# Performance work log

Measured on AMD Instinct MI355X. Metric: run time of the kernel, lower is better.

The kernel has to match this reference:

```python
import jax, jax.numpy as jnp
import numpy as np

M = 65536   # query points
N = 65536   # key points
K = 16      # neighbors per query
C = 64      # channels


def setup_inputs() -> dict:
    key = jax.random.key(0)
    ks = jax.random.split(key, 12)
    f = jax.random.normal
    s = 1.0 / np.sqrt(C).astype(np.float32)
    return {
        "q": f(ks[0], (M, C), dtype=jnp.float32),
        "k": f(ks[1], (N, C), dtype=jnp.float32),
        "value": f(ks[2], (M, K, C), dtype=jnp.float32),
        "q_pos": f(ks[3], (M, C), dtype=jnp.float32),
        "k_pos": f(ks[4], (N, C), dtype=jnp.float32),
        "mask": jax.random.uniform(ks[5], (M, K, 1)) < 0.1,
        "knearest_idx": jax.random.randint(ks[6], (2, M, K), 0, N),
        "k_num": K,
        # q_conv and k_conv share weights in the original module
        "Wqk": f(ks[7], (C, C), dtype=jnp.float32) * s,
        "bqk": jnp.zeros((C,), jnp.float32),
        "Wv": f(ks[8], (C, C), dtype=jnp.float32) * s,
        "bv": jnp.zeros((C,), jnp.float32),
        "Wg1": f(ks[9], (C, C), dtype=jnp.float32) * s,
        "bg1": jnp.zeros((C,), jnp.float32),
        "Wg2": f(ks[10], (C, C), dtype=jnp.float32) * s,
        "bg2": jnp.zeros((C,), jnp.float32),
        "Wt": f(ks[11], (C, C), dtype=jnp.float32) * s,
        "bt": jnp.zeros((C,), jnp.float32),
    }


def reference(q, k, value, q_pos, k_pos, mask, knearest_idx, k_num,
              Wqk, bqk, Wv, bv, Wg1, bg1, Wg2, bg2, Wt, bt):
    # shared q/k projection (tied weights) with positional add
    qp = (q + q_pos) @ Wqk + bqk            # [M, C]
    kp = (k + k_pos) @ Wqk + bqk            # [N, C]
    v = value @ Wv + bv                      # [M, K, C]
    # neighbor indices: row 1 of knearest_idx reshaped to [_, M, k_num]
    idx = knearest_idx.reshape(knearest_idx.shape[0], -1, k_num)[1]  # [M, K]
    kg = kp[idx]                              # gather -> [M, K, C]
    # per-edge MLP on q - k (fc_gamma)
    e = qp[:, None, :] - kg                   # [M, K, C]
    e = jax.nn.relu(e @ Wg1 + bg1) @ Wg2 + bg2
    e = jnp.where(mask, jnp.float32(-1e12), e)
    attn = jax.nn.softmax(e, axis=1)          # softmax over neighbor dim
    res = jnp.einsum('mnf,mnf->mf', attn, v)  # weighted aggregate -> [M, C]
    return res @ Wt + bt
```

## Files before the change

kernel.cpp:

```cpp
#include <hip/hip_runtime.h>
#include <hip/hip_bf16.h>

#define MQ 65536
#define NKEY 65536
#define KNB 16
#define CCH 64

typedef _Float16 half8  __attribute__((ext_vector_type(8)));
typedef _Float16 half4v __attribute__((ext_vector_type(4)));
typedef _Float16 half2v __attribute__((ext_vector_type(2)));
typedef float    floatx4 __attribute__((ext_vector_type(4)));


__global__ __launch_bounds__(256, 2)
void proj_prep(const float* __restrict__ q, const float* __restrict__ qpos,
               const float* __restrict__ k, const float* __restrict__ kpos,
               const float* __restrict__ Wqk, const float* __restrict__ bqk,
               const float* __restrict__ Wg1, const float* __restrict__ Wg2,
               const float* __restrict__ Wv,  const float* __restrict__ Wt,
               const unsigned char* __restrict__ maskraw,
               _Float16* __restrict__ qp_h, _Float16* __restrict__ kp_h,
               _Float16* __restrict__ w4, int* __restrict__ mflag)
{
    const int tid = threadIdx.x;

    if (blockIdx.x == 512) {
        __shared__ int sflags;
        if (tid == 0) sflags = 0;
        __syncthreads();
        const uint4* m4 = (const uint4*)maskraw;
        unsigned int orw = 0;
        #pragma unroll
        for (int it = 0; it < 4; ++it) {
            uint4 v = m4[tid + it * 256];
            orw |= v.x | v.y | v.z | v.w;
        }
        int local = 0;
        if (orw & 0x000000FFu) local |= 1;
        if (orw & 0x0000FF00u) local |= 2;
        if (orw & 0xFFFF0000u) local |= 4;
        if (local) atomicOr(&sflags, local);
        __syncthreads();
        if (tid == 0) *mflag = sflags;
        const float* Ws[4] = {Wg1, Wg2, Wv, Wt};
        #pragma unroll
        for (int mat = 0; mat < 4; ++mat) {
            const float* W = Ws[mat];
            _Float16* dst = w4 + mat * 64 * 72;
            for (int i = tid; i < 4096; i += 256) {
                int rr = i >> 6, c = i & 63;
                dst[c * 72 + rr] = (_Float16)W[i];
            }
        }
        return;
    }

    __shared__ __align__(16) _Float16 A_s[256 * 72];
    __shared__ __align__(16) _Float16 WT_s[64 * 72];

    const int r0 = blockIdx.x * 256;
    const float* x; const float* p; _Float16* o; int rb;
    if (r0 < MQ) { x = q; p = qpos; o = qp_h; rb = r0; }
    else         { x = k; p = kpos; o = kp_h; rb = r0 - MQ; }

    #pragma unroll
    for (int j = 0; j < 4; ++j) {
        int i = (tid + j * 256) * 4;
        int rr = i >> 6, c4 = i & 63;
        floatx4 wv = *(const floatx4*)&Wqk[rr * 64 + c4];
        WT_s[(c4 + 0) * 72 + rr] = (_Float16)wv.x;
        WT_s[(c4 + 1) * 72 + rr] = (_Float16)wv.y;
        WT_s[(c4 + 2) * 72 + rr] = (_Float16)wv.z;
        WT_s[(c4 + 3) * 72 + rr] = (_Float16)wv.w;
    }
    #pragma unroll
    for (int j = 0; j < 16; ++j) {
        int flat = tid + j * 256;
        int rr = flat >> 4, c4 = (flat & 15) * 4;
        size_t g = (size_t)(rb + rr) * 64 + c4;
        floatx4 xv = *(const floatx4*)&x[g];
        floatx4 pv = *(const floatx4*)&p[g];
        half4v h;
        h[0] = (_Float16)(xv.x + pv.x); h[1] = (_Float16)(xv.y + pv.y);
        h[2] = (_Float16)(xv.z + pv.z); h[3] = (_Float16)(xv.w + pv.w);
        *(half4v*)&A_s[rr * 72 + c4] = h;
    }
    __syncthreads();

    const int w = tid >> 6, lane = tid & 63, m = lane & 15, qd = lane >> 4;
    const floatx4 fz = {0.f, 0.f, 0.f, 0.f};
    floatx4 acc[4][4];
    #pragma unroll
    for (int rt = 0; rt < 4; rt++)
        #pragma unroll
        for (int ct = 0; ct < 4; ct++) acc[rt][ct] = fz;

    #pragma unroll
    for (int kc = 0; kc < 2; ++kc) {
        const int k0 = kc * 32 + qd * 8;
        half8 b[4];
        #pragma unroll
        for (int ct = 0; ct < 4; ++ct)
            b[ct] = *(const half8*)&WT_s[(ct * 16 + m) * 72 + k0];
        #pragma unroll
        for (int rt = 0; rt < 4; ++rt) {
            half8 a = *(const half8*)&A_s[(w * 64 + rt * 16 + m) * 72 + k0];
            #pragma unroll
            for (int ct = 0; ct < 4; ++ct)
                acc[rt][ct] = __builtin_amdgcn_mfma_f32_16x16x32_f16(a, b[ct], acc[rt][ct], 0, 0, 0);
        }
    }
    #pragma unroll
    for (int rt = 0; rt < 4; rt++) {
        #pragma unroll
        for (int ct = 0; ct < 4; ct++) {
            const int col = ct * 16 + m;
            const float bb = bqk[col];
            #pragma unroll
            for (int rg = 0; rg < 4; ++rg) {
                const int row = w * 64 + rt * 16 + qd * 4 + rg;
                A_s[row * 72 + col] = (_Float16)(acc[rt][ct][rg] + bb);
            }
        }
    }
    __syncthreads();
    #pragma unroll
    for (int j = 0; j < 8; ++j) {
        int ch = tid + j * 256;
        int rr = ch >> 3, off = (ch & 7) * 8;
        *(half8*)&o[(size_t)(rb + rr) * 64 + off] = *(const half8*)&A_s[rr * 72 + off];
    }
}

__global__ __launch_bounds__(256, 2)
void cross_attn(const float* __restrict__ value, const unsigned char* __restrict__ maskraw,
                const int* __restrict__ mflag, const int* __restrict__ idx,
                const _Float16* __restrict__ qp_h, const _Float16* __restrict__ kp_h,
                const _Float16* __restrict__ w4,
                const float* __restrict__ bg1, const float* __restrict__ bg2,
                const float* __restrict__ bv,  const float* __restrict__ bt,
                float* __restrict__ out)
{
    __shared__ __align__(16) _Float16 W4_s[4 * 64 * 72];
    __shared__ __align__(16) _Float16 D_s[256 * 72];
    __shared__ __align__(16) _Float16 res_s[16 * 72];
    __shared__ unsigned char mask_s[256];

    const int tid = threadIdx.x;
    const int q0 = blockIdx.x * 16;
    const int w = tid >> 6, lane = tid & 63, m = lane & 15, qd = lane >> 4;

    floatx4 vraw[16];
    {
        const size_t base = ((size_t)q0 * KNB + w * 64) * 64;
        #pragma unroll
        for (int rt = 0; rt < 4; ++rt)
            #pragma unroll
            for (int kc = 0; kc < 2; ++kc) {
                const float* vr = value + base + (size_t)(rt * 16 + m) * 64 + kc * 32 + qd * 8;
                vraw[(rt * 2 + kc) * 2 + 0] = *(const floatx4*)vr;
                vraw[(rt * 2 + kc) * 2 + 1] = *(const floatx4*)(vr + 4);
            }
    }

    #pragma unroll
    for (int j = 0; j < 9; ++j) {
        int ch = tid + j * 256;
        *(half8*)&W4_s[ch * 8] = *(const half8*)&w4[ch * 8];
    }
    {
        const int mode = *mflag;
        const size_t ei = (size_t)q0 * KNB + tid;
        unsigned char mv;
        if (mode & 2)      mv = maskraw[ei];
        else if (mode & 1) mv = ((const int*)maskraw)[ei] ? 1 : 0;
        else               mv = (((const float*)maskraw)[ei] != 0.f) ? 1 : 0;
        mask_s[tid] = mv;
    }
    {
        const int pr = tid & 31;
        #pragma unroll 8
        for (int i = 0; i < 32; ++i) {
            int e = (tid >> 5) + i * 8;
            int nb = idx[(size_t)q0 * KNB + e];
            int mrow = q0 + (e >> 4);
            half2v qv = *(const half2v*)&qp_h[(size_t)mrow * 64 + pr * 2];
            half2v kv = *(const half2v*)&kp_h[(size_t)nb * 64 + pr * 2];
            half2v d; d[0] = qv[0] - kv[0]; d[1] = qv[1] - kv[1];
            *(half2v*)&D_s[e * 72 + pr * 2] = d;
        }
    }
    __syncthreads();

    const floatx4 fz = {0.f, 0.f, 0.f, 0.f};
    float bvv[4], bg1v[4], bg2v[4];
    #pragma unroll
    for (int ct = 0; ct < 4; ct++) {
        const int col = ct * 16 + m;
        bvv[ct] = bv[col]; bg1v[ct] = bg1[col]; bg2v[ct] = bg2[col];
    }

    const _Float16* Wg1T = W4_s;
    const _Float16* Wg2T = W4_s + 4608;
    const _Float16* WvT  = W4_s + 2 * 4608;
    const _Float16* WtT  = W4_s + 3 * 4608;

    floatx4 acce[4][4];
    #pragma unroll
    for (int rt = 0; rt < 4; rt++)
        #pragma unroll
        for (int ct = 0; ct < 4; ct++) acce[rt][ct] = fz;
    #pragma unroll
    for (int kc = 0; kc < 2; ++kc) {
        const int k0 = kc * 32 + qd * 8;
        half8 b[4];
        #pragma unroll
        for (int ct = 0; ct < 4; ++ct)
            b[ct] = *(const half8*)&Wg1T[(ct * 16 + m) * 72 + k0];
        #pragma unroll
        for (int rt = 0; rt < 4; ++rt) {
            half8 a = *(const half8*)&D_s[(w * 64 + rt * 16 + m) * 72 + k0];
            #pragma unroll
            for (int ct = 0; ct < 4; ++ct)
                acce[rt][ct] = __builtin_amdgcn_mfma_f32_16x16x32_f16(a, b[ct], acce[rt][ct], 0, 0, 0);
        }
    }
    __syncthreads();
    #pragma unroll
    for (int rt = 0; rt < 4; rt++)
        #pragma unroll
        for (int ct = 0; ct < 4; ct++) {
            const int col = ct * 16 + m;
            #pragma unroll
            for (int rg = 0; rg < 4; ++rg) {
                const int row = w * 64 + rt * 16 + qd * 4 + rg;
                float h = acce[rt][ct][rg] + bg1v[ct];
                D_s[row * 72 + col] = (_Float16)fmaxf(h, 0.f);
            }
        }
    __syncthreads();

    #pragma unroll
    for (int rt = 0; rt < 4; rt++)
        #pragma unroll
        for (int ct = 0; ct < 4; ct++) acce[rt][ct] = fz;
    #pragma unroll
    for (int kc = 0; kc < 2; ++kc) {
        const int k0 = kc * 32 + qd * 8;
        half8 b[4];
        #pragma unroll
        for (int ct = 0; ct < 4; ++ct)
            b[ct] = *(const half8*)&Wg2T[(ct * 16 + m) * 72 + k0];
        #pragma unroll
        for (int rt = 0; rt < 4; ++rt) {
            half8 a = *(const half8*)&D_s[(w * 64 + rt * 16 + m) * 72 + k0];
            #pragma unroll
            for (int ct = 0; ct < 4; ++ct)
                acce[rt][ct] = __builtin_amdgcn_mfma_f32_16x16x32_f16(a, b[ct], acce[rt][ct], 0, 0, 0);
        }
    }

    half8 vfrag[8];
    #pragma unroll
    for (int f = 0; f < 8; ++f) {
        floatx4 x0 = vraw[f * 2], x1 = vraw[f * 2 + 1];
        half8 a;
        #pragma unroll
        for (int j = 0; j < 4; ++j) { a[j] = (_Float16)x0[j]; a[4 + j] = (_Float16)x1[j]; }
        vfrag[f] = a;
    }
    floatx4 accv[4][4];
    #pragma unroll
    for (int rt = 0; rt < 4; rt++)
        #pragma unroll
        for (int ct = 0; ct < 4; ct++) accv[rt][ct] = fz;
    #pragma unroll
    for (int kc = 0; kc < 2; ++kc) {
        const int k0 = kc * 32 + qd * 8;
        half8 b[4];
        #pragma unroll
        for (int ct = 0; ct < 4; ++ct)
            b[ct] = *(const half8*)&WvT[(ct * 16 + m) * 72 + k0];
        #pragma unroll
        for (int rt = 0; rt < 4; ++rt) {
            half8 a = vfrag[rt * 2 + kc];
            #pragma unroll
            for (int ct = 0; ct < 4; ++ct)
                accv[rt][ct] = __builtin_amdgcn_mfma_f32_16x16x32_f16(a, b[ct], accv[rt][ct], 0, 0, 0);
        }
    }

    #pragma unroll
    for (int rt = 0; rt < 4; rt++) {
        #pragma unroll
        for (int ct = 0; ct < 4; ct++) {
            float ev[4];
            #pragma unroll
            for (int rg = 0; rg < 4; ++rg) {
                const int erow = w * 64 + rt * 16 + qd * 4 + rg;
                float e = acce[rt][ct][rg] + bg2v[ct];
                ev[rg] = mask_s[erow] ? -1e12f : e;
            }
            float mx = fmaxf(fmaxf(ev[0], ev[1]), fmaxf(ev[2], ev[3]));
            mx = fmaxf(mx, __shfl_xor(mx, 16));
            mx = fmaxf(mx, __shfl_xor(mx, 32));
            float p[4], s = 0.f;
            #pragma unroll
            for (int rg = 0; rg < 4; ++rg) { p[rg] = __expf(ev[rg] - mx); s += p[rg]; }
            s += __shfl_xor(s, 16);
            s += __shfl_xor(s, 32);
            const float inv = 1.f / s;
            float t = 0.f;
            #pragma unroll
            for (int rg = 0; rg < 4; ++rg)
                t += p[rg] * inv * (accv[rt][ct][rg] + bvv[ct]);
            t += __shfl_xor(t, 16);
            t += __shfl_xor(t, 32);
            if (lane < 16) res_s[(w * 4 + rt) * 72 + ct * 16 + m] = (_Float16)t;
        }
    }
    __syncthreads();

    if (w == 0) {
        floatx4 acco[4] = {fz, fz, fz, fz};
        #pragma unroll
        for (int kc = 0; kc < 2; ++kc) {
            const int k0 = kc * 32 + qd * 8;
            half8 a = *(const half8*)&res_s[m * 72 + k0];
            #pragma unroll
            for (int ct = 0; ct < 4; ++ct) {
                half8 b = *(const half8*)&WtT[(ct * 16 + m) * 72 + k0];
                acco[ct] = __builtin_amdgcn_mfma_f32_16x16x32_f16(a, b, acco[ct], 0, 0, 0);
            }
        }
        #pragma unroll
        for (int ct = 0; ct < 4; ++ct) {
            const int col = ct * 16 + m;
            const float bb = bt[col];
            #pragma unroll
            for (int rg = 0; rg < 4; ++rg) {
                const int row = qd * 4 + rg;
                out[(size_t)(q0 + row) * 64 + col] = acco[ct][rg] + bb;
            }
        }
    }
}

extern "C" void kernel_launch(void* const* d_in, const int* in_sizes, int n_in,
                              void* d_out, int out_size, void* d_ws, size_t ws_size,
                              hipStream_t stream) {
    const float* q     = (const float*)d_in[0];
    const float* k     = (const float*)d_in[1];
    const float* value = (const float*)d_in[2];
    const float* q_pos = (const float*)d_in[3];
    const float* k_pos = (const float*)d_in[4];
    const unsigned char* mask = (const unsigned char*)d_in[5];
    const int* knn     = (const int*)d_in[6];
    const float* Wqk = (const float*)d_in[8];
    const float* bqk = (const float*)d_in[9];
    const float* Wv  = (const float*)d_in[10];
    const float* bv  = (const float*)d_in[11];
    const float* Wg1 = (const float*)d_in[12];
    const float* bg1 = (const float*)d_in[13];
    const float* Wg2 = (const float*)d_in[14];
    const float* bg2 = (const float*)d_in[15];
    const float* Wt  = (const float*)d_in[16];
    const float* bt  = (const float*)d_in[17];
    float* out = (float*)d_out;

    _Float16* qp_h = (_Float16*)d_ws;
    _Float16* kp_h = qp_h + (size_t)MQ * CCH;
    _Float16* w4   = kp_h + (size_t)NKEY * CCH;
    int* mflag     = (int*)(w4 + 4 * 64 * 72);
    const int* idx = knn + (size_t)MQ * KNB;

    proj_prep<<<513, 256, 0, stream>>>(q, q_pos, k, k_pos, Wqk, bqk,
                                       Wg1, Wg2, Wv, Wt, mask,
                                       qp_h, kp_h, w4, mflag);
    cross_attn<<<MQ / 16, 256, 0, stream>>>(value, mask, mflag, idx, qp_h, kp_h, w4,
                                            bg1, bg2, bv, bt, out);
}
```

Baseline: 538.0 us.

## Make cross-attention persistent over tiles with register prefetch and split out projection

New measurement: 683.6 us. +27.1%, slower.

```diff
diff --git a/kernel.cpp b/kernel.cpp
--- a/kernel.cpp
+++ b/kernel.cpp
@@ -5,60 +5,98 @@
 #define NKEY 65536
 #define KNB 16
 #define CCH 64
+#define TPB 8
 
 typedef _Float16 half8  __attribute__((ext_vector_type(8)));
 typedef _Float16 half4v __attribute__((ext_vector_type(4)));
-typedef _Float16 half2v __attribute__((ext_vector_type(2)));
 typedef float    floatx4 __attribute__((ext_vector_type(4)));
 
 
-__global__ __launch_bounds__(256, 2)
+__global__ void detect_mask(const unsigned char* __restrict__ m, int* __restrict__ flag)
+{
+    __shared__ int sflags;
+    if (threadIdx.x == 0) sflags = 0;
+    __syncthreads();
+    const uint4* m4 = (const uint4*)m;
+    unsigned int orw = 0;
+    #pragma unroll
+    for (int it = 0; it < 4; ++it) {
+        uint4 v = m4[threadIdx.x + it * 256];
+        orw |= v.x | v.y | v.z | v.w;
+    }
+    int local = 0;
+    if (orw & 0x000000FFu) local |= 1;
+    if (orw & 0x0000FF00u) local |= 2;
+    if (orw & 0xFFFF0000u) local |= 4;
+    if (local) atomicOr(&sflags, local);
+    __syncthreads();
+    if (threadIdx.x == 0) *flag = sflags;
+}
+
+__global__ __launch_bounds__(256, 4)
 void proj_prep(const float* __restrict__ q, const float* __restrict__ qpos,
                const float* __restrict__ k, const float* __restrict__ kpos,
                const float* __restrict__ Wqk, const float* __restrict__ bqk,
                const float* __restrict__ Wg1, const float* __restrict__ Wg2,
                const float* __restrict__ Wv,  const float* __restrict__ Wt,
-               const unsigned char* __restrict__ maskraw,
+               const unsigned char* __restrict__ maskraw, const int* __restrict__ mflag,
                _Float16* __restrict__ qp_h, _Float16* __restrict__ kp_h,
-               _Float16* __restrict__ w4, int* __restrict__ mflag)
+               _Float16* __restrict__ w4, unsigned short* __restrict__ mask_packed)
 {
     const int tid = threadIdx.x;
-
-    if (blockIdx.x == 512) {
-        __shared__ int sflags;
-        if (tid == 0) sflags = 0;
-        __syncthreads();
-        const uint4* m4 = (const uint4*)maskraw;
-        unsigned int orw = 0;
-        #pragma unroll
-        for (int it = 0; it < 4; ++it) {
-            uint4 v = m4[tid + it * 256];
-            orw |= v.x | v.y | v.z | v.w;
-        }
-        int local = 0;
-        if (orw & 0x000000FFu) local |= 1;
-        if (orw & 0x0000FF00u) local |= 2;
-        if (orw & 0xFFFF0000u) local |= 4;
-        if (local) atomicOr(&sflags, local);
-        __syncthreads();
-        if (tid == 0) *mflag = sflags;
-        const float* Ws[4] = {Wg1, Wg2, Wv, Wt};
-        #pragma unroll
-        for (int mat = 0; mat < 4; ++mat) {
-            const float* W = Ws[mat];
-            _Float16* dst = w4 + mat * 64 * 72;
-            for (int i = tid; i < 4096; i += 256) {
-                int rr = i >> 6, c = i & 63;
-                dst[c * 72 + rr] = (_Float16)W[i];
+    const int bid = blockIdx.x;
+
+    if (bid >= 1024) {
+        if (bid < 1088) {
+            const int mode = *mflag;
+            const int qq0 = (bid - 1024) * 1024 + tid * 4;
+            unsigned short mp[4];
+            #pragma unroll
+            for (int i = 0; i < 4; ++i) {
+                const int qq = qq0 + i;
+                unsigned bits = 0;
+                if (mode & 2) {
+                    uint4 v = ((const uint4*)maskraw)[qq];
+                    unsigned wds[4] = {v.x, v.y, v.z, v.w};
+                    #pragma unroll
+                    for (int wi = 0; wi < 4; ++wi)
+                        #pragma unroll
+                        for (int b = 0; b < 4; ++b)
+                            if ((wds[wi] >> (8 * b)) & 0xFFu) bits |= 1u << (wi * 4 + b);
+                } else {
+                    const uint4* p = (const uint4*)maskraw + (size_t)qq * 4;
+                    #pragma unroll
+                    for (int wi = 0; wi < 4; ++wi) {
+                        uint4 v = p[wi];
+                        bits |= (v.x ? 1u : 0u) << (wi * 4 + 0);
+                        bits |= (v.y ? 1u : 0u) << (wi * 4 + 1);
+                        bits |= (v.z ? 1u : 0u) << (wi * 4 + 2);
+                        bits |= (v.w ? 1u : 0u) << (wi * 4 + 3);
+                    }
+                }
+                mp[i] = (unsigned short)bits;
+            }
+            ushort4 o4; o4.x = mp[0]; o4.y = mp[1]; o4.z = mp[2]; o4.w = mp[3];
+            *(ushort4*)&mask_packed[qq0] = o4;
+        } else {
+            const float* Ws[4] = {Wg1, Wg2, Wv, Wt};
+            #pragma unroll
+            for (int mat = 0; mat < 4; ++mat) {
+                const float* W = Ws[mat];
+                _Float16* dst = w4 + mat * 64 * 72;
+                for (int i = tid; i < 4096; i += 256) {
+                    int rr = i >> 6, c = i & 63;
+                    dst[c * 72 + rr] = (_Float16)W[i];
+                }
             }
         }
         return;
     }
 
-    __shared__ __align__(16) _Float16 A_s[256 * 72];
+    __shared__ __align__(16) _Float16 A_s[128 * 72];
     __shared__ __align__(16) _Float16 WT_s[64 * 72];
 
-    const int r0 = blockIdx.x * 256;
+    const int r0 = bid * 128;
     const float* x; const float* p; _Float16* o; int rb;
     if (r0 < MQ) { x = q; p = qpos; o = qp_h; rb = r0; }
     else         { x = k; p = kpos; o = kp_h; rb = r0 - MQ; }
@@ -67,14 +105,14 @@
     for (int j = 0; j < 4; ++j) {
         int i = (tid + j * 256) * 4;
         int rr = i >> 6, c4 = i & 63;
-        floatx4 wv = *(const floatx4*)&Wqk[rr * 64 + c4];
+        floatx4 wv = *(const floatx4*)&Wqk[i];
         WT_s[(c4 + 0) * 72 + rr] = (_Float16)wv.x;
         WT_s[(c4 + 1) * 72 + rr] = (_Float16)wv.y;
         WT_s[(c4 + 2) * 72 + rr] = (_Float16)wv.z;
         WT_s[(c4 + 3) * 72 + rr] = (_Float16)wv.w;
     }
     #pragma unroll
-    for (int j = 0; j < 16; ++j) {
+    for (int j = 0; j < 8; ++j) {
         int flat = tid + j * 256;
         int rr = flat >> 4, c4 = (flat & 15) * 4;
         size_t g = (size_t)(rb + rr) * 64 + c4;
@@ -89,9 +127,9 @@
 
     const int w = tid >> 6, lane = tid & 63, m = lane & 15, qd = lane >> 4;
     const floatx4 fz = {0.f, 0.f, 0.f, 0.f};
-    floatx4 acc[4][4];
-    #pragma unroll
-    for (int rt = 0; rt < 4; rt++)
+    floatx4 acc[2][4];
+    #pragma unroll
+    for (int rt = 0; rt < 2; rt++)
         #pragma unroll
         for (int ct = 0; ct < 4; ct++) acc[rt][ct] = fz;
 
@@ -103,29 +141,28 @@
         for (int ct = 0; ct < 4; ++ct)
             b[ct] = *(const half8*)&WT_s[(ct * 16 + m) * 72 + k0];
         #pragma unroll
-        for (int rt = 0; rt < 4; ++rt) {
-            half8 a = *(const half8*)&A_s[(w * 64 + rt * 16 + m) * 72 + k0];
+        for (int rt = 0; rt < 2; ++rt) {
+            half8 a = *(const half8*)&A_s[(w * 32 + rt * 16 + m) * 72 + k0];
             #pragma unroll
             for (int ct = 0; ct < 4; ++ct)
                 acc[rt][ct] = __builtin_amdgcn_mfma_f32_16x16x32_f16(a, b[ct], acc[rt][ct], 0, 0, 0);
         }
     }
     #pragma unroll
-    for (int rt = 0; rt < 4; rt++) {
+    for (int rt = 0; rt < 2; rt++)
         #pragma unroll
         for (int ct = 0; ct < 4; ct++) {
             const int col = ct * 16 + m;
             const float bb = bqk[col];
             #pragma unroll
             for (int rg = 0; rg < 4; ++rg) {
-                const int row = w * 64 + rt * 16 + qd * 4 + rg;
+                const int row = w * 32 + rt * 16 + qd * 4 + rg;
                 A_s[row * 72 + col] = (_Float16)(acc[rt][ct][rg] + bb);
             }
         }
-    }
-    __syncthreads();
-    #pragma unroll
-    for (int j = 0; j < 8; ++j) {
+    __syncthreads();
+    #pragma unroll
+    for (int j = 0; j < 4; ++j) {
         int ch = tid + j * 256;
         int rr = ch >> 3, off = (ch & 7) * 8;
         *(half8*)&o[(size_t)(rb + rr) * 64 + off] = *(const half8*)&A_s[rr * 72 + off];
@@ -133,215 +170,257 @@
 }
 
 __global__ __launch_bounds__(256, 2)
-void cross_attn(const float* __restrict__ value, const unsigned char* __restrict__ maskraw,
-                const int* __restrict__ mflag, const int* __restrict__ idx,
+void cross_attn(const float* __restrict__ value, const unsigned short* __restrict__ mask_packed,
+                const int* __restrict__ idx,
                 const _Float16* __restrict__ qp_h, const _Float16* __restrict__ kp_h,
                 const _Float16* __restrict__ w4,
                 const float* __restrict__ bg1, const float* __restrict__ bg2,
-                const float* __restrict__ bv,  const float* __restrict__ bt,
-                float* __restrict__ out)
+                const float* __restrict__ bv,
+                _Float16* __restrict__ res_g)
 {
-    __shared__ __align__(16) _Float16 W4_s[4 * 64 * 72];
-    __shared__ __align__(16) _Float16 D_s[256 * 72];
-    __shared__ __align__(16) _Float16 res_s[16 * 72];
-    __shared__ unsigned char mask_s[256];
-
-    const int tid = threadIdx.x;
-    const int q0 = blockIdx.x * 16;
-    const int w = tid >> 6, lane = tid & 63, m = lane & 15, qd = lane >> 4;
-
+    __shared__ __align__(16) _Float16 W3_s[3 * 64 * 72];
+    __shared__ __align__(16) _Float16 H_s[256 * 72];
+
+    const int tid = threadIdx.x, w = tid >> 6, lane = tid & 63, m = lane & 15, qd = tid >> 4 & 3;
+    const int tile0 = blockIdx.x * TPB;
+
+    for (int ch = tid; ch < 1728; ch += 256)
+        *(half8*)&W3_s[ch * 8] = *(const half8*)&w4[ch * 8];
+
+    float bg1v[4], bg2v[4], bvv[4];
+    #pragma unroll
+    for (int ct = 0; ct < 4; ct++) {
+        const int col = ct * 16 + m;
+        bg1v[ct] = bg1[col]; bg2v[ct] = bg2[col]; bvv[ct] = bv[col];
+    }
+
+    int idxr[4]; unsigned mpr[4];
+    half8 qpr[4][2], kpr[4][2];
     floatx4 vraw[16];
     {
-        const size_t base = ((size_t)q0 * KNB + w * 64) * 64;
-        #pragma unroll
-        for (int rt = 0; rt < 4; ++rt)
+        const int q0 = tile0 * 16;
+        #pragma unroll
+        for (int rt = 0; rt < 4; ++rt) {
+            const int qrow = q0 + w * 4 + rt;
+            idxr[rt] = idx[qrow * KNB + m];
+            mpr[rt]  = mask_packed[qrow];
+            #pragma unroll
+            for (int kc = 0; kc < 2; ++kc)
+                qpr[rt][kc] = *(const half8*)&qp_h[(size_t)qrow * 64 + kc * 32 + qd * 8];
             #pragma unroll
             for (int kc = 0; kc < 2; ++kc) {
-                const float* vr = value + base + (size_t)(rt * 16 + m) * 64 + kc * 32 + qd * 8;
+                const float* vr = value + ((size_t)qrow * KNB + m) * 64 + kc * 32 + qd * 8;
                 vraw[(rt * 2 + kc) * 2 + 0] = *(const floatx4*)vr;
                 vraw[(rt * 2 + kc) * 2 + 1] = *(const floatx4*)(vr + 4);
             }
-    }
-
-    #pragma unroll
-    for (int j = 0; j < 9; ++j) {
-        int ch = tid + j * 256;
-        *(half8*)&W4_s[ch * 8] = *(const half8*)&w4[ch * 8];
-    }
-    {
-        const int mode = *mflag;
-        const size_t ei = (size_t)q0 * KNB + tid;
-        unsigned char mv;
-        if (mode & 2)      mv = maskraw[ei];
-        else if (mode & 1) mv = ((const int*)maskraw)[ei] ? 1 : 0;
-        else               mv = (((const float*)maskraw)[ei] != 0.f) ? 1 : 0;
-        mask_s[tid] = mv;
-    }
-    {
-        const int pr = tid & 31;
-        #pragma unroll 8
-        for (int i = 0; i < 32; ++i) {
-            int e = (tid >> 5) + i * 8;
-            int nb = idx[(size_t)q0 * KNB + e];
-            int mrow = q0 + (e >> 4);
-            half2v qv = *(const half2v*)&qp_h[(size_t)mrow * 64 + pr * 2];
-            half2v kv = *(const half2v*)&kp_h[(size_t)nb * 64 + pr * 2];
-            half2v d; d[0] = qv[0] - kv[0]; d[1] = qv[1] - kv[1];
-            *(half2v*)&D_s[e * 72 + pr * 2] = d;
-        }
-    }
-    __syncthreads();
-
+        }
+        #pragma unroll
+        for (int rt = 0; rt < 4; ++rt)
+            #pragma unroll
+            for (int kc = 0; kc < 2; ++kc)
+                kpr[rt][kc] = *(const half8*)&kp_h[(size_t)idxr[rt] * 64 + kc * 32 + qd * 8];
+    }
+    __syncthreads();
+
+    const _Float16* Wg1T = W3_s;
+    const _Float16* Wg2T = W3_s + 4608;
+    const _Float16* WvT  = W3_s + 2 * 4608;
     const floatx4 fz = {0.f, 0.f, 0.f, 0.f};
-    float bvv[4], bg1v[4], bg2v[4];
-    #pragma unroll
-    for (int ct = 0; ct < 4; ct++) {
-        const int col = ct * 16 + m;
-        bvv[ct] = bv[col]; bg1v[ct] = bg1[col]; bg2v[ct] = bg2[col];
-    }
-
-    const _Float16* Wg1T = W4_s;
-    const _Float16* Wg2T = W4_s + 4608;
-    const _Float16* WvT  = W4_s + 2 * 4608;
-    const _Float16* WtT  = W4_s + 3 * 4608;
-
-    floatx4 acce[4][4];
-    #pragma unroll
-    for (int rt = 0; rt < 4; rt++)
-        #pragma unroll
-        for (int ct = 0; ct < 4; ct++) acce[rt][ct] = fz;
-    #pragma unroll
-    for (int kc = 0; kc < 2; ++kc) {
-        const int k0 = kc * 32 + qd * 8;
-        half8 b[4];
-        #pragma unroll
-        for (int ct = 0; ct < 4; ++ct)
-            b[ct] = *(const half8*)&Wg1T[(ct * 16 + m) * 72 + k0];
-        #pragma unroll
-        for (int rt = 0; rt < 4; ++rt) {
-            half8 a = *(const half8*)&D_s[(w * 64 + rt * 16 + m) * 72 + k0];
-            #pragma unroll
-            for (int ct = 0; ct < 4; ++ct)
-                acce[rt][ct] = __builtin_amdgcn_mfma_f32_16x16x32_f16(a, b[ct], acce[rt][ct], 0, 0, 0);
-        }
-    }
-    __syncthreads();
-    #pragma unroll
-    for (int rt = 0; rt < 4; rt++)
-        #pragma unroll
-        for (int ct = 0; ct < 4; ct++) {
-            const int col = ct * 16 + m;
-            #pragma unroll
-            for (int rg = 0; rg < 4; ++rg) {
-                const int row = w * 64 + rt * 16 + qd * 4 + rg;
-                float h = acce[rt][ct][rg] + bg1v[ct];
-                D_s[row * 72 + col] = (_Float16)fmaxf(h, 0.f);
-            }
-        }
-    __syncthreads();
-
-    #pragma unroll
-    for (int rt = 0; rt < 4; rt++)
-        #pragma unroll
-        for (int ct = 0; ct < 4; ct++) acce[rt][ct] = fz;
-    #pragma unroll
-    for (int kc = 0; kc < 2; ++kc) {
-        const int k0 = kc * 32 + qd * 8;
-        half8 b[4];
-        #pragma unroll
-        for (int ct = 0; ct < 4; ++ct)
-            b[ct] = *(const half8*)&Wg2T[(ct * 16 + m) * 72 + k0];
-        #pragma unroll
-        for (int rt = 0; rt < 4; ++rt) {
-            half8 a = *(const half8*)&D_s[(w * 64 + rt * 16 + m) * 72 + k0];
-            #pragma unroll
-            for (int ct = 0; ct < 4; ++ct)
-                acce[rt][ct] = __builtin_amdgcn_mfma_f32_16x16x32_f16(a, b[ct], acce[rt][ct], 0, 0, 0);
-        }
-    }
-
-    half8 vfrag[8];
-    #pragma unroll
-    for (int f = 0; f < 8; ++f) {
-        floatx4 x0 = vraw[f * 2], x1 = vraw[f * 2 + 1];
-        half8 a;
-        #pragma unroll
-        for (int j = 0; j < 4; ++j) { a[j] = (_Float16)x0[j]; a[4 + j] = (_Float16)x1[j]; }
-        vfrag[f] = a;
-    }
-    floatx4 accv[4][4];
-    #pragma unroll
-    for (int rt = 0; rt < 4; rt++)
-        #pragma unroll
-        for (int ct = 0; ct < 4; ct++) accv[rt][ct] = fz;
-    #pragma unroll
-    for (int kc = 0; kc < 2; ++kc) {
-        const int k0 = kc * 32 + qd * 8;
-        half8 b[4];
-        #pragma unroll
-        for (int ct = 0; ct < 4; ++ct)
-            b[ct] = *(const half8*)&WvT[(ct * 16 + m) * 72 + k0];
-        #pragma unroll
-        for (int rt = 0; rt < 4; ++rt) {
-            half8 a = vfrag[rt * 2 + kc];
-            #pragma unroll
-            for (int ct = 0; ct < 4; ++ct)
-                accv[rt][ct] = __builtin_amdgcn_mfma_f32_16x16x32_f16(a, b[ct], accv[rt][ct], 0, 0, 0);
-        }
-    }
-
-    #pragma unroll
-    for (int rt = 0; rt < 4; rt++) {
-        #pragma unroll
-        for (int ct = 0; ct < 4; ct++) {
-            float ev[4];
-            #pragma unroll
-            for (int rg = 0; rg < 4; ++rg) {
-                const int erow = w * 64 + rt * 16 + qd * 4 + rg;
-                float e = acce[rt][ct][rg] + bg2v[ct];
-                ev[rg] = mask_s[erow] ? -1e12f : e;
-            }
-            float mx = fmaxf(fmaxf(ev[0], ev[1]), fmaxf(ev[2], ev[3]));
-            mx = fmaxf(mx, __shfl_xor(mx, 16));
-            mx = fmaxf(mx, __shfl_xor(mx, 32));
-            float p[4], s = 0.f;
-            #pragma unroll
-            for (int rg = 0; rg < 4; ++rg) { p[rg] = __expf(ev[rg] - mx); s += p[rg]; }
-            s += __shfl_xor(s, 16);
-            s += __shfl_xor(s, 32);
-            const float inv = 1.f / s;
-            float t = 0.f;
-            #pragma unroll
-            for (int rg = 0; rg < 4; ++rg)
-                t += p[rg] * inv * (accv[rt][ct][rg] + bvv[ct]);
-            t += __shfl_xor(t, 16);
-            t += __shfl_xor(t, 32);
-            if (lane < 16) res_s[(w * 4 + rt) * 72 + ct * 16 + m] = (_Float16)t;
-        }
-    }
-    __syncthreads();
-
-    if (w == 0) {
-        floatx4 acco[4] = {fz, fz, fz, fz};
+
+    for (int t = 0; t < TPB; ++t) {
+        const int q0t = (tile0 + t) * 16;
+        const bool more = (t + 1 < TPB);
+        unsigned mcur[4];
+        #pragma unroll
+        for (int rt = 0; rt < 4; ++rt) mcur[rt] = mpr[rt];
+
+        half8 vfrag[8];
+        #pragma unroll
+        for (int f = 0; f < 8; ++f) {
+            floatx4 x0 = vraw[f * 2], x1 = vraw[f * 2 + 1];
+            half8 a;
+            #pragma unroll
+            for (int j = 0; j < 4; ++j) { a[j] = (_Float16)x0[j]; a[4 + j] = (_Float16)x1[j]; }
+            vfrag[f] = a;
+        }
+
+        floatx4 acch[4][4];
+        #pragma unroll
+        for (int rt = 0; rt < 4; rt++)
+            #pragma unroll
+            for (int ct = 0; ct < 4; ct++) acch[rt][ct] = fz;
         #pragma unroll
         for (int kc = 0; kc < 2; ++kc) {
             const int k0 = kc * 32 + qd * 8;
-            half8 a = *(const half8*)&res_s[m * 72 + k0];
-            #pragma unroll
-            for (int ct = 0; ct < 4; ++ct) {
-                half8 b = *(const half8*)&WtT[(ct * 16 + m) * 72 + k0];
-                acco[ct] = __builtin_amdgcn_mfma_f32_16x16x32_f16(a, b, acco[ct], 0, 0, 0);
-            }
+            half8 b[4];
+            #pragma unroll
+            for (int ct = 0; ct < 4; ++ct)
+                b[ct] = *(const half8*)&Wg1T[(ct * 16 + m) * 72 + k0];
+            #pragma unroll
+            for (int rt = 0; rt < 4; ++rt) {
+                half8 a = qpr[rt][kc] - kpr[rt][kc];
+                #pragma unroll
+                for (int ct = 0; ct < 4; ++ct)
+                    acch[rt][ct] = __builtin_amdgcn_mfma_f32_16x16x32_f16(a, b[ct], acch[rt][ct], 0, 0, 0);
+            }
+        }
+
+        int idxn[4];
+        if (more) {
+            const int q0n = (tile0 + t + 1) * 16;
+            #pragma unroll
+            for (int rt = 0; rt < 4; ++rt) {
+                const int qrow = q0n + w * 4 + rt;
+                idxn[rt] = idx[qrow * KNB + m];
+                mpr[rt]  = mask_packed[qrow];
+                #pragma unroll
+                for (int kc = 0; kc < 2; ++kc)
+                    qpr[rt][kc] = *(const half8*)&qp_h[(size_t)qrow * 64 + kc * 32 + qd * 8];
+                #pragma unroll
+                for (int kc = 0; kc < 2; ++kc) {
+                    const float* vr = value + ((size_t)qrow * KNB + m) * 64 + kc * 32 + qd * 8;
+                    vraw[(rt * 2 + kc) * 2 + 0] = *(const floatx4*)vr;
+                    vraw[(rt * 2 + kc) * 2 + 1] = *(const floatx4*)(vr + 4);
+                }
+            }
+        }
+
+        #pragma unroll
+        for (int rt = 0; rt < 4; rt++)
+            #pragma unroll
+            for (int ct = 0; ct < 4; ct++) {
+                const int col = ct * 16 + m;
+                #pragma unroll
+                for (int rg = 0; rg < 4; ++rg) {
+                    const int row = w * 64 + rt * 16 + qd * 4 + rg;
+                    float h = acch[rt][ct][rg] + bg1v[ct];
+                    H_s[row * 72 + col] = (_Float16)fmaxf(h, 0.f);
+                }
+            }
+        __asm__ volatile("s_waitcnt lgkmcnt(0)" ::: "memory");
+
+        floatx4 acce[4][4];
+        #pragma unroll
+        for (int rt = 0; rt < 4; rt++)
+            #pragma unroll
+            for (int ct = 0; ct < 4; ct++) acce[rt][ct] = fz;
+        #pragma unroll
+        for (int kc = 0; kc < 2; ++kc) {
+            const int k0 = kc * 32 + qd * 8;
+            half8 b[4];
+            #pragma unroll
+            for (int ct = 0; ct < 4; ++ct)
+                b[ct] = *(const half8*)&Wg2T[(ct * 16 + m) * 72 + k0];
+            #pragma unroll
+            for (int rt = 0; rt < 4; ++rt) {
+                half8 a = *(const half8*)&H_s[(w * 64 + rt * 16 + m) * 72 + k0];
+                #pragma unroll
+                for (int ct = 0; ct < 4; ++ct)
+                    acce[rt][ct] = __builtin_amdgcn_mfma_f32_16x16x32_f16(a, b[ct], acce[rt][ct], 0, 0, 0);
+            }
+        }
+
+        if (more) {
+            #pragma unroll
+            for (int rt = 0; rt < 4; ++rt)
+                #pragma unroll
+                for (int kc = 0; kc < 2; ++kc)
+                    kpr[rt][kc] = *(const half8*)&kp_h[(size_t)idxn[rt] * 64 + kc * 32 + qd * 8];
+        }
+
+        floatx4 accv[4][4];
+        #pragma unroll
+        for (int rt = 0; rt < 4; rt++)
+            #pragma unroll
+            for (int ct = 0; ct < 4; ct++) accv[rt][ct] = fz;
+        #pragma unroll
+        for (int kc = 0; kc < 2; ++kc) {
+            const int k0 = kc * 32 + qd * 8;
+            half8 b[4];
+            #pragma unroll
+            for (int ct = 0; ct < 4; ++ct)
+                b[ct] = *(const half8*)&WvT[(ct * 16 + m) * 72 + k0];
+            #pragma unroll
+            for (int rt = 0; rt < 4; ++rt) {
+                half8 a = vfrag[rt * 2 + kc];
+                #pragma unroll
+                for (int ct = 0; ct < 4; ++ct)
+                    accv[rt][ct] = __builtin_amdgcn_mfma_f32_16x16x32_f16(a, b[ct], accv[rt][ct], 0, 0, 0);
+            }
+        }
+
+        #pragma unroll
+        for (int rt = 0; rt < 4; rt++) {
+            float tca[4];
+            #pragma unroll
+            for (int ct = 0; ct < 4; ct++) {
+                float ev[4];
+                #pragma unroll
+                for (int rg = 0; rg < 4; ++rg) {
+                    float e = acce[rt][ct][rg] + bg2v[ct];
+                    ev[rg] = ((mcur[rt] >> (qd * 4 + rg)) & 1u) ? -1e12f : e;
+                }
+                float mx = fmaxf(fmaxf(ev[0], ev[1]), fmaxf(ev[2], ev[3]));
+                mx = fmaxf(mx, __shfl_xor(mx, 16));
+                mx = fmaxf(mx, __shfl_xor(mx, 32));
+                float pp[4], s = 0.f;
+                #pragma unroll
+                for (int rg = 0; rg < 4; ++rg) { pp[rg] = __expf(ev[rg] - mx); s += pp[rg]; }
+                s += __shfl_xor(s, 16);
+                s += __shfl_xor(s, 32);
+                const float inv = 1.f / s;
+                float tt = 0.f;
+                #pragma unroll
+                for (int rg = 0; rg < 4; ++rg)
+                    tt += pp[rg] * inv * (accv[rt][ct][rg] + bvv[ct]);
+                tt += __shfl_xor(tt, 16);
+                tt += __shfl_xor(tt, 32);
+                tca[ct] = tt;
+            }
+            float tsel = (qd == 0) ? tca[0] : (qd == 1) ? tca[1] : (qd == 2) ? tca[2] : tca[3];
+            res_g[(size_t)(q0t + w * 4 + rt) * 64 + lane] = (_Float16)tsel;
+        }
+    }
+}
+
+__global__ __launch_bounds__(256, 4)
+void out_proj(const _Float16* __restrict__ res_g, const _Float16* __restrict__ w4,
+              const float* __restrict__ bt, float* __restrict__ out)
+{
+    __shared__ __align__(16) _Float16 WtT_s[64 * 72];
+    const int tid = threadIdx.x;
+    const _Float16* WtT_g = w4 + 3 * 4608;
+    for (int ch = tid; ch < 576; ch += 256)
+        *(half8*)&WtT_s[ch * 8] = *(const half8*)&WtT_g[ch * 8];
+    __syncthreads();
+
+    const int w = tid >> 6, lane = tid & 63, m = lane & 15, qd = lane >> 4;
+    const int rb = blockIdx.x * 256;
+    const floatx4 fz = {0.f, 0.f, 0.f, 0.f};
+    float btv[4];
+    #pragma unroll
+    for (int ct = 0; ct < 4; ++ct) btv[ct] = bt[ct * 16 + m];
+
+    #pragma unroll
+    for (int rt = 0; rt < 4; ++rt) {
+        floatx4 acc[4] = {fz, fz, fz, fz};
+        #pragma unroll
+        for (int kc = 0; kc < 2; ++kc) {
+            const int k0 = kc * 32 + qd * 8;
+            half8 a = *(const half8*)&res_g[(size_t)(rb + w * 64 + rt * 16 + m) * 64 + k0];
+            half8 b[4];
+            #pragma unroll
+            for (int ct = 0; ct < 4; ++ct)
+                b[ct] = *(const half8*)&WtT_s[(ct * 16 + m) * 72 + k0];
+            #pragma unroll
+            for (int ct = 0; ct < 4; ++ct)
+                acc[ct] = __builtin_amdgcn_mfma_f32_16x16x32_f16(a, b[ct], acc[ct], 0, 0, 0);
         }
         #pragma unroll
         for (int ct = 0; ct < 4; ++ct) {
-            const int col = ct * 16 + m;
-            const float bb = bt[col];
-            #pragma unroll
-            for (int rg = 0; rg < 4; ++rg) {
-                const int row = qd * 4 + rg;
-                out[(size_t)(q0 + row) * 64 + col] = acco[ct][rg] + bb;
-            }
+            #pragma unroll
+            for (int rg = 0; rg < 4; ++rg)
+                out[(size_t)(rb + w * 64 + rt * 16 + qd * 4 + rg) * 64 + ct * 16 + m] = acc[ct][rg] + btv[ct];
         }
     }
 }
@@ -368,15 +447,19 @@
     const float* bt  = (const float*)d_in[17];
     float* out = (float*)d_out;
 
-    _Float16* qp_h = (_Float16*)d_ws;
-    _Float16* kp_h = qp_h + (size_t)MQ * CCH;
-    _Float16* w4   = kp_h + (size_t)NKEY * CCH;
-    int* mflag     = (int*)(w4 + 4 * 64 * 72);
+    _Float16* qp_h  = (_Float16*)d_ws;
+    _Float16* kp_h  = qp_h + (size_t)MQ * CCH;
+    _Float16* res_g = kp_h + (size_t)NKEY * CCH;
+    _Float16* w4    = res_g + (size_t)MQ * CCH;
+    unsigned short* mask_packed = (unsigned short*)(w4 + 4 * 64 * 72);
+    int* mflag = (int*)(mask_packed + MQ);
     const int* idx = knn + (size_t)MQ * KNB;
 
-    proj_prep<<<513, 256, 0, stream>>>(q, q_pos, k, k_pos, Wqk, bqk,
-                                       Wg1, Wg2, Wv, Wt, mask,
-                                       qp_h, kp_h, w4, mflag);
-    cross_attn<<<MQ / 16, 256, 0, stream>>>(value, mask, mflag, idx, qp_h, kp_h, w4,
-                                            bg1, bg2, bv, bt, out);
+    detect_mask<<<1, 256, 0, stream>>>(mask, mflag);
+    proj_prep<<<1089, 256, 0, stream>>>(q, q_pos, k, k_pos, Wqk, bqk,
+                                        Wg1, Wg2, Wv, Wt, mask, mflag,
+                                        qp_h, kp_h, w4, mask_packed);
+    cross_attn<<<MQ / (16 * TPB), 256, 0, stream>>>(value, mask_packed, idx, qp_h, kp_h, w4,
+                                                    bg1, bg2, bv, res_g);
+    out_proj<<<MQ / 256, 256, 0, stream>>>(res_g, w4, bt, out);
 }
```
